# Kernel optimization log

Hardware: AMD Instinct MI355X
Metric: run time of the kernel (lower is better)

The kernel has to match this reference:

```python
import jax, jax.numpy as jnp
import numpy as np

NUM_HEADS = 8
DIM = 384


def conv2d(x, w, padding, groups=1):
    return jax.lax.conv_general_dilated(
        x, w, window_strides=(1, 1), padding=[(padding, padding), (padding, padding)],
        feature_group_count=groups, dimension_numbers=("NCHW", "OIHW", "NCHW"))


def setup_inputs() -> dict:
    key = jax.random.key(0)
    ks = jax.random.split(key, 6)
    d = DIM
    x = jax.random.normal(ks[0], (4, d, 128, 128), dtype=jnp.float32)
    w_qkv = jax.random.normal(ks[1], (3 * d, d, 1, 1), dtype=jnp.float32) * 0.05
    w_dw = jax.random.normal(ks[2], (3 * d, 1, 3, 3), dtype=jnp.float32) * 0.05
    w_proj = jax.random.normal(ks[3], (d, 2 * d, 1, 1), dtype=jnp.float32) * 0.05
    w_bs_pw = jax.random.normal(ks[4], (d, d, 1, 1), dtype=jnp.float32) * 0.05
    w_bs_dw = jax.random.normal(ks[5], (d, 1, 3, 3), dtype=jnp.float32) * 0.05
    return {"x": x, "w_qkv": w_qkv, "w_dw": w_dw, "w_proj": w_proj,
            "w_bs_pw": w_bs_pw, "w_bs_dw": w_bs_dw}


def reference(x, w_qkv, w_dw, w_proj, w_bs_pw, w_bs_dw):
    b, c, h, w = x.shape
    ch = c // NUM_HEADS
    # BSConvU branch: pointwise 1x1 then depthwise 3x3, then exact GELU
    y = conv2d(x, w_bs_pw, padding=0)
    y = conv2d(y, w_bs_dw, padding=1, groups=c)
    y = jax.nn.gelu(y, approximate=False)
    # qkv: 1x1 conv then depthwise 3x3
    qkv = conv2d(x, w_qkv, padding=0)
    qkv = conv2d(qkv, w_dw, padding=1, groups=3 * c)
    q, k, v = jnp.split(qkv, 3, axis=1)
    # b (head ch) h w -> b head ch (h w)
    def to_heads(t):
        return t.reshape(b, NUM_HEADS, ch, h * w)
    q, k, v = to_heads(q), to_heads(k), to_heads(v)
    # L2-normalize over spatial dim (torch F.normalize with eps=1e-12)
    q = q / jnp.maximum(jnp.linalg.norm(q, axis=-1, keepdims=True), 1e-12)
    k = k / jnp.maximum(jnp.linalg.norm(k, axis=-1, keepdims=True), 1e-12)
    scale = 1.0 / np.sqrt(ch).astype(np.float32)
    attn = jnp.einsum("bhcn,bhdn->bhcd", q, k) * scale  # channel-channel attention
    attn = jax.nn.softmax(attn, axis=-1)
    out = jnp.einsum("bhcd,bhdn->bhcn", attn, v)
    out = out.reshape(b, c, h, w)
    out = jnp.concatenate([out, y], axis=1)
    out = conv2d(out, w_proj, padding=0)
    return out
```

## Files before the change

### kernel.cpp

```cpp
#include <hip/hip_runtime.h>
#include <hip/hip_bf16.h>
#include <math.h>

typedef __hip_bfloat16 bf16;
typedef short bf16x8 __attribute__((ext_vector_type(8)));
typedef float f32x4 __attribute__((ext_vector_type(4)));

#define NPIX 16384

static __device__ __forceinline__ float ldv(float v) { return v; }
static __device__ __forceinline__ float ldv(bf16 v) { return __bfloat162float(v); }
static __device__ __forceinline__ float lds16(short s) {
    union { short s_; bf16 h; } u; u.s_ = s; return __bfloat162float(u.h);
}
template <typename T> static __device__ __forceinline__ T stv(float v);
template <> __device__ __forceinline__ float stv<float>(float v) { return v; }
template <> __device__ __forceinline__ bf16 stv<bf16>(float v) { return __float2bfloat16(v); }
static __device__ __forceinline__ short stv16(float v) {
    union { short s_; bf16 h; } u; u.h = __float2bfloat16(v); return u.s_;
}

static __device__ __forceinline__ unsigned pack2f(float a, float b) {
    union { bf16 h; unsigned short u; } ua, ub;
    ua.h = __float2bfloat16(a); ub.h = __float2bfloat16(b);
    return (unsigned)ua.u | ((unsigned)ub.u << 16);
}
static __device__ __forceinline__ unsigned packbb(unsigned short lo, unsigned short hi) {
    return (unsigned)lo | ((unsigned)hi << 16);
}

template <typename SrcT>
static __device__ __forceinline__ const SrcT* maprow(const SrcT* A, const SrcT* B, int k,
    int Ksplit, int agrp, int ags, int abss, int bgrp, int bgs, int bbs, int b)
{
    if (k < Ksplit) return A + (size_t)((k / agrp) * ags + b * abss + (k % agrp)) * NPIX;
    k -= Ksplit;
    return B + (size_t)((k / bgrp) * bgs + b * bbs + (k % bgrp)) * NPIX;
}

__global__ __launch_bounds__(256) void packw(const float* __restrict__ s,
                                             bf16* __restrict__ d, int n)
{
    int i = (blockIdx.x * 256 + threadIdx.x) * 8;
    if (i + 8 > n) return;
    float4 v0 = *(const float4*)(s + i);
    float4 v1 = *(const float4*)(s + i + 4);
    uint4 u;
    u.x = pack2f(v0.x, v0.y); u.y = pack2f(v0.z, v0.w);
    u.z = pack2f(v1.x, v1.y); u.w = pack2f(v1.z, v1.w);
    *(uint4*)(void*)(d + i) = u;
}

__global__ __launch_bounds__(256) void xpose(const float* __restrict__ x,
                                             bf16* __restrict__ xT)
{
    __shared__ short Ls[64 * 384];
    const int t = threadIdx.x;
    const int px0 = blockIdx.x * 64;
    const int b = blockIdx.y;
    const float* xb = x + (size_t)b * 384 * NPIX;

#pragma unroll 4
    for (int i = 0; i < 24; ++i) {
        int e = i * 256 + t;
        int ch = e >> 4, seg = e & 15;
        float4 v = *(const float4*)(xb + (size_t)ch * NPIX + px0 + seg * 4);
        const float* vp = (const float*)&v;
#pragma unroll
        for (int j = 0; j < 4; ++j) {
            int px = seg * 4 + j;
            int B = (ch >> 3) ^ ((px >> 2) & 7);
            Ls[px * 384 + B * 8 + (ch & 7)] = stv16(vp[j]);
        }
    }
    __syncthreads();

    const int lpx = t >> 2;
    const int m = (lpx >> 2) & 7;
    bf16* ob = xT + ((size_t)b * NPIX + px0 + lpx) * 384;
#pragma unroll
    for (int j = 0; j < 12; ++j) {
        int B = (t & 3) + j * 4;
        bf16x8 blk = *(const bf16x8*)&Ls[lpx * 384 + (B ^ m) * 8];
        *(bf16x8*)(void*)(ob + B * 8) = blk;
    }
}

__global__ __launch_bounds__(256) void xposeB(const bf16* __restrict__ src,
                                              bf16* __restrict__ dst)
{
    __shared__ short Ls[64 * 384];
    const int t = threadIdx.x;
    const int px0 = blockIdx.x * 64;
    const int b = blockIdx.y;
    const bf16* sb = src + (size_t)b * 384 * NPIX;

#pragma unroll 4
    for (int i = 0; i < 12; ++i) {
        int e = i * 256 + t;
        int ch = e >> 3, seg = e & 7;
        bf16x8 v = *(const bf16x8*)(const void*)(sb + (size_t)ch * NPIX + px0 + seg * 8);
#pragma unroll
        for (int j = 0; j < 8; ++j) {
            int px = seg * 8 + j;
            int B = (ch >> 3) ^ ((px >> 2) & 7);
            Ls[px * 384 + B * 8 + (ch & 7)] = v[j];
        }
    }
    __syncthreads();

    const int lpx = t >> 2;
    const int m = (lpx >> 2) & 7;
    bf16* ob = dst + ((size_t)b * NPIX + px0 + lpx) * 768 + 384;
#pragma unroll
    for (int j = 0; j < 12; ++j) {
        int B = (t & 3) + j * 4;
        bf16x8 blk = *(const bf16x8*)&Ls[lpx * 384 + (B ^ m) * 8];
        *(bf16x8*)(void*)(ob + B * 8) = blk;
    }
}

template <int BM, int K, typename OutT>
__global__ __launch_bounds__(256) void gemm3(
    const bf16* __restrict__ wp, int G, int wsA, int wrowMul,
    const bf16* __restrict__ bsrc,
    OutT* __restrict__ out, int osA, int obS,
    int bmCount, int nwg)
{
    constexpr int MT = BM / 16;
    constexpr int S  = K / 32;
    constexpr int ACH = BM * 4;
    __shared__ __align__(16) short As[2][BM * 40];
    __shared__ __align__(16) short Bs[2][128 * 40];

    const int t = threadIdx.x;
    const int gid = blockIdx.x;
    const int w = (gid & 7) * (nwg >> 3) + (gid >> 3);
    const int bm = w % bmCount, grp = w / bmCount;
    const int b = grp & 3, px0 = (grp >> 2) * 128;

    const int l = t & 63, wvid = t >> 6, l15 = l & 15, q = l >> 4;
    const int wr0 = bm * wrowMul;
    const size_t bRow0 = (size_t)b * NPIX + px0;

    const int e0 = t,        r0 = e0 >> 2, c0 = e0 & 3;
    const int e1 = t + 256,  r1 = e1 >> 2, c1 = e1 & 3;
    const bf16* apt0 = wp + (size_t)(wr0 + (r0 / G) * wsA + (r0 % G)) * K + c0 * 8;
    const bf16* apt1 = wp + (size_t)(wr0 + (r1 / G) * wsA + (r1 % G)) * K + c1 * 8;
    const int sA0 = r0 * 40 + c0 * 8, sA1 = r1 * 40 + c1 * 8;
    const bf16* apt2 = apt0; int sA2 = sA0; bool has2 = false;
    if constexpr (ACH > 512) {
        if (t < ACH - 512) {
            int e2 = t + 512, r2 = e2 >> 2, c2 = e2 & 3;
            apt2 = wp + (size_t)(wr0 + (r2 / G) * wsA + (r2 % G)) * K + c2 * 8;
            sA2 = r2 * 40 + c2 * 8;
            has2 = true;
        }
    }
    const bf16* bpt0 = bsrc + (bRow0 + r0) * K + c0 * 8;
    const bf16* bpt1 = bsrc + (bRow0 + r1) * K + c1 * 8;

    f32x4 acc[MT][2];
#pragma unroll
    for (int mt = 0; mt < MT; ++mt)
#pragma unroll
        for (int nt = 0; nt < 2; ++nt) acc[mt][nt] = (f32x4){0.f, 0.f, 0.f, 0.f};

    bf16x8 aR0, aR1, aR2, bR0, bR1;

    auto GLOADS = [&](int kk) {
        aR0 = *(const bf16x8*)(const void*)(apt0 + kk);
        aR1 = *(const bf16x8*)(const void*)(apt1 + kk);
        if constexpr (ACH > 512) { if (has2) aR2 = *(const bf16x8*)(const void*)(apt2 + kk); }
        bR0 = *(const bf16x8*)(const void*)(bpt0 + kk);
        bR1 = *(const bf16x8*)(const void*)(bpt1 + kk);
    };
    auto SSTORES = [&](int buf) {
        *(bf16x8*)&As[buf][sA0] = aR0;
        *(bf16x8*)&As[buf][sA1] = aR1;
        if constexpr (ACH > 512) { if (has2) *(bf16x8*)&As[buf][sA2] = aR2; }
        *(bf16x8*)&Bs[buf][sA0] = bR0;
        *(bf16x8*)&Bs[buf][sA1] = bR1;
    };

    GLOADS(0);
    SSTORES(0);
    __syncthreads();

#pragma unroll
    for (int s = 0; s < S; ++s) {
        const int cur = s & 1;
        if (s + 1 < S) GLOADS((s + 1) * 32);
        bf16x8 af[MT], bfv[2];
#pragma unroll
        for (int mt = 0; mt < MT; ++mt)
            af[mt] = *(const bf16x8*)&As[cur][(mt * 16 + l15) * 40 + q * 8];
#pragma unroll
        for (int nt = 0; nt < 2; ++nt)
            bfv[nt] = *(const bf16x8*)&Bs[cur][(wvid * 32 + nt * 16 + l15) * 40 + q * 8];
#pragma unroll
        for (int mt = 0; mt < MT; ++mt)
#pragma unroll
            for (int nt = 0; nt < 2; ++nt)
                acc[mt][nt] = __builtin_amdgcn_mfma_f32_16x16x32_bf16(
                    af[mt], bfv[nt], acc[mt][nt], 0, 0, 0);
        if (s + 1 < S) SSTORES(1 - cur);
        __syncthreads();
    }

    const int obase = bm * osA + b * obS;
#pragma unroll
    for (int mt = 0; mt < MT; ++mt)
#pragma unroll
        for (int nt = 0; nt < 2; ++nt)
#pragma unroll
            for (int r = 0; r < 4; ++r) {
                int row = obase + mt * 16 + q * 4 + r;
                int col = px0 + wvid * 32 + nt * 16 + l15;
                out[(size_t)row * NPIX + col] = stv<OutT>(acc[mt][nt][r]);
            }
}

template <typename SrcT, typename OutT>
__global__ __launch_bounds__(256) void gemm48(
    const SrcT* __restrict__ srcA, const SrcT* __restrict__ srcB, int Ksplit, int K,
    int agrp, int ags, int abss, int bgrp, int bgs, int bbs,
    const float* __restrict__ w, int wMod, int wsA, int wsB, int wrow0,
    OutT* __restrict__ out, int oMod, int osA, int osB, int obS, int orow0)
{
    __shared__ __align__(16) short As[2][48 * 40];
    __shared__ __align__(16) short Bs[2][128 * 40];

    const int t  = threadIdx.x;
    const int bm = blockIdx.x;
    const int p0 = blockIdx.y * 128;
    const int b  = blockIdx.z;

    const int l = t & 63, wvid = t >> 6, l15 = l & 15, q = l >> 4;
    const int c4 = t >> 4, rp = t & 15;

    const int wbase = wrow0 + (bm % wMod) * wsA + (bm / wMod) * wsB;

    f32x4 acc[3][2];
#pragma unroll
    for (int mt = 0; mt < 3; ++mt)
#pragma unroll
        for (int nt = 0; nt < 2; ++nt) acc[mt][nt] = (f32x4){0.f, 0.f, 0.f, 0.f};

    float aw[6];
    float fb[16];
    bf16x8 hA, hB;

    auto LOADA = [&](int k0) {
#pragma unroll
        for (int i = 0; i < 3; ++i) {
            int idx = t + i * 256, row = idx >> 4, kq = idx & 15;
            float2 v = *(const float2*)(w + (size_t)(wbase + row) * K + k0 + kq * 2);
            aw[2 * i] = v.x; aw[2 * i + 1] = v.y;
        }
    };
    auto STOREA = [&](int buf) {
#pragma unroll
        for (int i = 0; i < 3; ++i) {
            int idx = t + i * 256, row = idx >> 4, kq = idx & 15;
            *(unsigned*)&As[buf][row * 40 + kq * 2] = pack2f(aw[2 * i], aw[2 * i + 1]);
        }
    };
    auto LOADB = [&](int k0) {
        const SrcT* r0 = maprow(srcA, srcB, k0 + 2 * rp,     Ksplit, agrp, ags, abss, bgrp, bgs, bbs, b) + p0 + c4 * 8;
        const SrcT* r1 = maprow(srcA, srcB, k0 + 2 * rp + 1, Ksplit, agrp, ags, abss, bgrp, bgs, bbs, b) + p0 + c4 * 8;
        if constexpr (sizeof(SrcT) == 4) {
            float4 a0 = *(const float4*)r0, a1 = *(const float4*)(r0 + 4);
            float4 b0 = *(const float4*)r1, b1 = *(const float4*)(r1 + 4);
            fb[0] = a0.x; fb[1] = a0.y; fb[2] = a0.z; fb[3] = a0.w;
            fb[4] = a1.x; fb[5] = a1.y; fb[6] = a1.z; fb[7] = a1.w;
            fb[8] = b0.x; fb[9] = b0.y; fb[10] = b0.z; fb[11] = b0.w;
            fb[12] = b1.x; fb[13] = b1.y; fb[14] = b1.z; fb[15] = b1.w;
        } else {
            hA = *(const bf16x8*)(const void*)r0;
            hB = *(const bf16x8*)(const void*)r1;
        }
    };
    auto STOREB = [&](int buf) {
#pragma unroll
        for (int j = 0; j < 8; ++j) {
            unsigned d;
            if constexpr (sizeof(SrcT) == 4) d = pack2f(fb[j], fb[8 + j]);
            else d = packbb((unsigned short)hA[j], (unsigned short)hB[j]);
            *(unsigned*)&Bs[buf][(c4 * 8 + j) * 40 + rp * 2] = d;
        }
    };

    LOADA(0); LOADB(0);
    STOREA(0); STOREB(0);
    const int S = K / 32;
    for (int s = 0; s < S; ++s) {
        const int cur = s & 1;
        __syncthreads();
        if (s + 1 < S) { LOADA((s + 1) * 32); LOADB((s + 1) * 32); }
        bf16x8 af[3], bfr[2];
#pragma unroll
        for (int mt = 0; mt < 3; ++mt)
            af[mt] = *(const bf16x8*)&As[cur][(mt * 16 + l15) * 40 + q * 8];
#pragma unroll
        for (int nt = 0; nt < 2; ++nt)
            bfr[nt] = *(const bf16x8*)&Bs[cur][(wvid * 32 + nt * 16 + l15) * 40 + q * 8];
#pragma unroll
        for (int mt = 0; mt < 3; ++mt)
#pragma unroll
            for (int nt = 0; nt < 2; ++nt)
                acc[mt][nt] = __builtin_amdgcn_mfma_f32_16x16x32_bf16(
                    af[mt], bfr[nt], acc[mt][nt], 0, 0, 0);
        if (s + 1 < S) { STOREA(1 - cur); STOREB(1 - cur); }
    }

    const int obase = orow0 + (bm % oMod) * osA + (bm / oMod) * osB + b * obS;
#pragma unroll
    for (int mt = 0; mt < 3; ++mt)
#pragma unroll
        for (int nt = 0; nt < 2; ++nt)
#pragma unroll
            for (int r = 0; r < 4; ++r) {
                int row = obase + mt * 16 + q * 4 + r;
                int col = p0 + wvid * 32 + nt * 16 + l15;
                out[(size_t)row * NPIX + col] = stv<OutT>(acc[mt][nt][r]);
            }
}

__global__ __launch_bounds__(256) void dw3x3v(
    const bf16* __restrict__ in, const float* __restrict__ w, bf16* __restrict__ out,
    int isQkv, int whofs, int inB, int ig, int outB, int og, int obase, int applyGelu)
{
    const int t = threadIdx.x;
    const int g = blockIdx.x * 256 + t;
    const int c = blockIdx.y;
    const int b = blockIdx.z;
    const int y = g >> 4;
    const int x0 = (g & 15) * 8;

    int inRow, wch, outRow;
    if (isQkv) {
        int h = c / 144, r = c - h * 144;
        inRow  = h * ig + b * inB + r;
        wch    = (r / 48) * 384 + h * 48 + whofs + (r % 48);
        outRow = h * og + b * outB + r + obase;
    } else {
        inRow = b * inB + c; wch = c; outRow = b * outB + c;
    }

    const bf16* ib = in + (size_t)inRow * NPIX;
    float wv[9];
#pragma unroll
    for (int i = 0; i < 9; ++i) wv[i] = w[wch * 9 + i];

    float vv[3][10];
#pragma unroll
    for (int dy = 0; dy < 3; ++dy) {
        int yy = y + dy - 1;
        if (yy < 0 || yy > 127) {
#pragma unroll
            for (int j = 0; j < 10; ++j) vv[dy][j] = 0.f;
        } else {
            const bf16* rb = ib + yy * 128;
            bf16x8 m = *(const bf16x8*)(const void*)(rb + x0);
#pragma unroll
            for (int j = 0; j < 8; ++j) vv[dy][j + 1] = lds16(m[j]);
            vv[dy][0] = (x0 > 0)   ? ldv(rb[x0 - 1]) : 0.f;
            vv[dy][9] = (x0 < 120) ? ldv(rb[x0 + 8]) : 0.f;
        }
    }
    bf16x8 res;
#pragma unroll
    for (int j = 0; j < 8; ++j) {
        float a = 0.f;
#pragma unroll
        for (int dy = 0; dy < 3; ++dy)
#pragma unroll
            for (int dx = 0; dx < 3; ++dx)
                a += wv[dy * 3 + dx] * vv[dy][j + dx];
        if (applyGelu) a = 0.5f * a * (1.0f + erff(a * 0.70710678118654752f));
        res[j] = stv16(a);
    }
    *(bf16x8*)(void*)(out + (size_t)outRow * NPIX + y * 128 + x0) = res;
}

__global__ __launch_bounds__(256) void l2norm_v(const bf16* __restrict__ qkvd,
                                                float* __restrict__ inv, int NBH)
{
    const int id = blockIdx.x;
    const int which = id / (NBH * 48);
    const int rem = id - which * NBH * 48;
    const int bh = rem / 48, c = rem - bh * 48;
    const bf16* base = qkvd + (size_t)(bh * 144 + which * 48 + c) * NPIX;

    float s = 0.f;
#pragma unroll
    for (int it = 0; it < 8; ++it) {
        bf16x8 v = *(const bf16x8*)(const void*)(base + ((size_t)threadIdx.x + it * 256) * 8);
#pragma unroll
        for (int j = 0; j < 8; ++j) { float f = lds16(v[j]); s += f * f; }
    }
#pragma unroll
    for (int off = 32; off; off >>= 1) s += __shfl_down(s, off, 64);
    __shared__ float partial[4];
    if ((threadIdx.x & 63) == 0) partial[threadIdx.x >> 6] = s;
    __syncthreads();
    if (threadIdx.x == 0) {
        float tt = partial[0] + partial[1] + partial[2] + partial[3];
        inv[(which * NBH + bh) * 48 + c] = 1.0f / fmaxf(sqrtf(tt), 1e-12f);
    }
}

__global__ __launch_bounds__(256) void qk_mfma(const bf16* __restrict__ qkvd,
                                               float* __restrict__ lp, int NBH, int pxs)
{
    const int bh = blockIdx.x;
    const int wvid = threadIdx.x >> 6;
    const int slice = blockIdx.y * 4 + wvid;
    const int l = threadIdx.x & 63, l15 = l & 15, q = l >> 4;

    const bf16* qb = qkvd + (size_t)(bh * 144) * NPIX;
    const bf16* kb = qb + (size_t)48 * NPIX;

    f32x4 acc[3][3];
#pragma unroll
    for (int mt = 0; mt < 3; ++mt)
#pragma unroll
        for (int nt = 0; nt < 3; ++nt) acc[mt][nt] = (f32x4){0.f, 0.f, 0.f, 0.f};

    const int pbeg = slice * pxs;
    for (int kk = 0; kk < pxs; kk += 32) {
        const int pc = pbeg + kk + q * 8;
        bf16x8 af[3], bfv[3];
#pragma unroll
        for (int mt = 0; mt < 3; ++mt)
            af[mt] = *(const bf16x8*)(const void*)(qb + (size_t)(mt * 16 + l15) * NPIX + pc);
#pragma unroll
        for (int nt = 0; nt < 3; ++nt)
            bfv[nt] = *(const bf16x8*)(const void*)(kb + (size_t)(nt * 16 + l15) * NPIX + pc);
#pragma unroll
        for (int mt = 0; mt < 3; ++mt)
#pragma unroll
            for (int nt = 0; nt < 3; ++nt)
                acc[mt][nt] = __builtin_amdgcn_mfma_f32_16x16x32_bf16(
                    af[mt], bfv[nt], acc[mt][nt], 0, 0, 0);
    }
    float* o = lp + ((size_t)slice * NBH + bh) * 2304;
#pragma unroll
    for (int mt = 0; mt < 3; ++mt)
#pragma unroll
        for (int nt = 0; nt < 3; ++nt)
#pragma unroll
            for (int r = 0; r < 4; ++r)
                o[(mt * 16 + q * 4 + r) * 48 + nt * 16 + l15] = acc[mt][nt][r];
}

__global__ __launch_bounds__(256) void logit_reduce(const float* __restrict__ lp,
                                                    const float* __restrict__ inv,
                                                    float* __restrict__ L,
                                                    int NBH, int NSL)
{
    const int blk = blockIdx.x;
    const int bh = blk / 9, chunk = blk - bh * 9;
    const int e = chunk * 256 + threadIdx.x;
    float s = 0.f;
    for (int sl = 0; sl < NSL; ++sl)
        s += lp[((size_t)sl * NBH + bh) * 2304 + e];
    const int i = e / 48, j = e - i * 48;
    L[(size_t)bh * 2304 + e] =
        s * 0.14433756729740643f * inv[bh * 48 + i] * inv[(NBH + bh) * 48 + j];
}

__global__ __launch_bounds__(256) void softmax48b(const float* __restrict__ Lg,
                                                  bf16* __restrict__ a_bf)
{
    const int bh = blockIdx.x, t = threadIdx.x;
    __shared__ float L[2304];
    for (int e = t; e < 2304; e += 256) L[e] = Lg[(size_t)bh * 2304 + e];
    __syncthreads();
    if (t < 48) {
        float m = -1e30f;
#pragma unroll
        for (int j = 0; j < 48; ++j) m = fmaxf(m, L[t * 48 + j]);
        float e_[48]; float ssum = 0.f;
#pragma unroll
        for (int j = 0; j < 48; ++j) { e_[j] = expf(L[t * 48 + j] - m); ssum += e_[j]; }
        float r = 1.f / ssum;
        bf16* ab = a_bf + (size_t)bh * 3072 + t * 64;
#pragma unroll
        for (int j = 0; j < 48; ++j) ab[j] = stv<bf16>(e_[j] * r);
#pragma unroll
        for (int j = 48; j < 64; ++j) ab[j] = stv<bf16>(0.f);
    }
}

__global__ __launch_bounds__(256) void softmax48(const float* __restrict__ lp,
                                                 const float* __restrict__ inv,
                                                 bf16* __restrict__ a_bf, int NBH, int NSL)
{
    const int bh = blockIdx.x, t = threadIdx.x;
    __shared__ float L[2304];
    for (int e = t; e < 2304; e += 256) {
        float s = 0.f;
        for (int sl = 0; sl < NSL; ++sl) s += lp[((size_t)sl * NBH + bh) * 2304 + e];
        int i = e / 48, j = e - i * 48;
        L[e] = s * 0.14433756729740643f * inv[bh * 48 + i] * inv[(NBH + bh) * 48 + j];
    }
    __syncthreads();
    if (t < 48) {
        float m = -1e30f;
#pragma unroll
        for (int j = 0; j < 48; ++j) m = fmaxf(m, L[t * 48 + j]);
        float e_[48]; float ssum = 0.f;
#pragma unroll
        for (int j = 0; j < 48; ++j) { e_[j] = expf(L[t * 48 + j] - m); ssum += e_[j]; }
        float r = 1.f / ssum;
        bf16* ab = a_bf + (size_t)bh * 3072 + t * 64;
#pragma unroll
        for (int j = 0; j < 48; ++j) ab[j] = stv<bf16>(e_[j] * r);
#pragma unroll
        for (int j = 48; j < 64; ++j) ab[j] = stv<bf16>(0.f);
    }
}

__global__ __launch_bounds__(256) void av_mfma(const bf16* __restrict__ a_bf,
                                               const bf16* __restrict__ qkvd,
                                               bf16* __restrict__ out, int obase, int oS)
{
    __shared__ __align__(16) short Bs[128 * 72];
    const int t = threadIdx.x;
    const int px0 = blockIdx.x * 128;
    const int bh = blockIdx.y;
    const int l = t & 63, wvid = t >> 6, l15 = l & 15, q = l >> 4;
    const int c4 = t >> 4, rp = t & 15;

    const bf16* ab = a_bf + (size_t)bh * 3072;
    bf16x8 af[3][2];
#pragma unroll
    for (int mt = 0; mt < 3; ++mt)
#pragma unroll
        for (int kq = 0; kq < 2; ++kq)
            af[mt][kq] = *(const bf16x8*)(const void*)(ab + (mt * 16 + l15) * 64 + kq * 32 + q * 8);

    const bf16* vb = qkvd + (size_t)(bh * 144 + 96) * NPIX;
    bf16x8 vr[4];
#pragma unroll
    for (int jj = 0; jj < 4; ++jj) {
        int j = rp * 4 + jj; int jc = j < 48 ? j : 47;
        vr[jj] = *(const bf16x8*)(const void*)(vb + (size_t)jc * NPIX + px0 + c4 * 8);
    }
#pragma unroll
    for (int j = 0; j < 8; ++j) {
        *(unsigned*)&Bs[(c4 * 8 + j) * 72 + rp * 4]     = packbb((unsigned short)vr[0][j], (unsigned short)vr[1][j]);
        *(unsigned*)&Bs[(c4 * 8 + j) * 72 + rp * 4 + 2] = packbb((unsigned short)vr[2][j], (unsigned short)vr[3][j]);
    }
    __syncthreads();

    f32x4 acc[3][2];
#pragma unroll
    for (int mt = 0; mt < 3; ++mt)
#pragma unroll
        for (int nt = 0; nt < 2; ++nt) acc[mt][nt] = (f32x4){0.f, 0.f, 0.f, 0.f};

    bf16x8 bfv[2][2];
#pragma unroll
    for (int nt = 0; nt < 2; ++nt)
#pragma unroll
        for (int kq = 0; kq < 2; ++kq)
            bfv[nt][kq] = *(const bf16x8*)&Bs[(wvid * 32 + nt * 16 + l15) * 72 + kq * 32 + q * 8];
#pragma unroll
    for (int kq = 0; kq < 2; ++kq)
#pragma unroll
        for (int mt = 0; mt < 3; ++mt)
#pragma unroll
            for (int nt = 0; nt < 2; ++nt)
                acc[mt][nt] = __builtin_amdgcn_mfma_f32_16x16x32_bf16(
                    af[mt][kq], bfv[nt][kq], acc[mt][nt], 0, 0, 0);
#pragma unroll
    for (int mt = 0; mt < 3; ++mt)
#pragma unroll
        for (int nt = 0; nt < 2; ++nt)
#pragma unroll
            for (int r = 0; r < 4; ++r) {
                int row = obase + bh * oS + mt * 16 + q * 4 + r;
                int col = px0 + wvid * 32 + nt * 16 + l15;
                out[(size_t)row * NPIX + col] = stv<bf16>(acc[mt][nt][r]);
            }
}

__global__ __launch_bounds__(256) void av_mfma2(const bf16* __restrict__ a_bf,
                                                const bf16* __restrict__ qkvd,
                                                bf16* __restrict__ pxT)
{
    __shared__ __align__(16) short Bs[128 * 72];
    const int t = threadIdx.x;
    const int px0 = blockIdx.x * 128;
    const int bh = blockIdx.y;
    const int l = t & 63, wvid = t >> 6, l15 = l & 15, q = l >> 4;
    const int c4 = t >> 4, rp = t & 15;

    const bf16* ab = a_bf + (size_t)bh * 3072;
    bf16x8 af[3][2];
#pragma unroll
    for (int mt = 0; mt < 3; ++mt)
#pragma unroll
        for (int kq = 0; kq < 2; ++kq)
            af[mt][kq] = *(const bf16x8*)(const void*)(ab + (mt * 16 + l15) * 64 + kq * 32 + q * 8);

    const bf16* vb = qkvd + (size_t)(bh * 144 + 96) * NPIX;
    bf16x8 vr[4];
#pragma unroll
    for (int jj = 0; jj < 4; ++jj) {
        int j = rp * 4 + jj; int jc = j < 48 ? j : 47;
        vr[jj] = *(const bf16x8*)(const void*)(vb + (size_t)jc * NPIX + px0 + c4 * 8);
    }
#pragma unroll
    for (int j = 0; j < 8; ++j) {
        *(unsigned*)&Bs[(c4 * 8 + j) * 72 + rp * 4]     = packbb((unsigned short)vr[0][j], (unsigned short)vr[1][j]);
        *(unsigned*)&Bs[(c4 * 8 + j) * 72 + rp * 4 + 2] = packbb((unsigned short)vr[2][j], (unsigned short)vr[3][j]);
    }
    __syncthreads();

    f32x4 acc[3][2];
#pragma unroll
    for (int mt = 0; mt < 3; ++mt)
#pragma unroll
        for (int nt = 0; nt < 2; ++nt) acc[mt][nt] = (f32x4){0.f, 0.f, 0.f, 0.f};

    bf16x8 bfv[2][2];
#pragma unroll
    for (int nt = 0; nt < 2; ++nt)
#pragma unroll
        for (int kq = 0; kq < 2; ++kq)
            bfv[nt][kq] = *(const bf16x8*)&Bs[(wvid * 32 + nt * 16 + l15) * 72 + kq * 32 + q * 8];
#pragma unroll
    for (int kq = 0; kq < 2; ++kq)
#pragma unroll
        for (int mt = 0; mt < 3; ++mt)
#pragma unroll
            for (int nt = 0; nt < 2; ++nt)
                acc[mt][nt] = __builtin_amdgcn_mfma_f32_16x16x32_bf16(
                    af[mt][kq], bfv[nt][kq], acc[mt][nt], 0, 0, 0);

    __syncthreads();
#pragma unroll
    for (int mt = 0; mt < 3; ++mt)
#pragma unroll
        for (int nt = 0; nt < 2; ++nt) {
            int pxl = wvid * 32 + nt * 16 + l15;
#pragma unroll
            for (int r = 0; r < 2; ++r)
                *(unsigned*)&Bs[pxl * 48 + mt * 16 + q * 4 + r * 2] =
                    pack2f(acc[mt][nt][2 * r], acc[mt][nt][2 * r + 1]);
        }
    __syncthreads();

    const int h = bh >> 2, bb = bh & 3;
    const int pxl = t >> 1, half = t & 1;
    bf16* ob = pxT + ((size_t)bb * NPIX + px0 + pxl) * 768 + h * 48 + half * 24;
#pragma unroll
    for (int j = 0; j < 3; ++j)
        *(bf16x8*)(void*)(ob + j * 8) = *(const bf16x8*)&Bs[pxl * 48 + half * 24 + j * 8];
}

extern "C" void kernel_launch(void* const* d_in, const int* in_sizes, int n_in,
                              void* d_out, int out_size, void* d_ws, size_t ws_size,
                              hipStream_t stream) {
    const float* x       = (const float*)d_in[0];
    const float* w_qkv   = (const float*)d_in[1];
    const float* w_dw    = (const float*)d_in[2];
    const float* w_proj  = (const float*)d_in[3];
    const float* w_bs_pw = (const float*)d_in[4];
    const float* w_bs_dw = (const float*)d_in[5];
    float* out = (float*)d_out;
    bf16* y1 = (bf16*)d_out;

    const size_t SZQ = 150994944ull;
    const size_t SZH = 18874368ull;
    const size_t SZY = 50331648ull;
    const size_t SZPXT = 100663296ull;
    char* ws = (char*)d_ws;
    dim3 blk(256);

    if (ws_size >= 371404800ull) {
        bf16* qkvp = (bf16*)ws;
        bf16* pxT  = (bf16*)ws;
        bf16* wprojp = (bf16*)(ws + SZPXT);
        float* Lbuf  = (float*)(ws + SZPXT + 1048576ull);
        bf16* qkvd = (bf16*)(ws + SZQ);
        bf16* xT   = (bf16*)(ws + 2 * SZQ);
        bf16* yg   = xT;
        float* lp  = (float*)(ws + 2 * SZQ + SZY);
        bf16* wqkvp = (bf16*)lp;
        bf16* wbsp  = (bf16*)((char*)lp + 884736ull);
        bf16* abf  = (bf16*)(ws + 2 * SZQ + SZY + 18874368ull);
        float* inv = (float*)(ws + 2 * SZQ + SZY + 18874368ull + 196608ull);

        packw<<<dim3(216), blk, 0, stream>>>(w_qkv, wqkvp, 442368);
        packw<<<dim3(72), blk, 0, stream>>>(w_bs_pw, wbsp, 147456);
        xpose<<<dim3(256, 4), blk, 0, stream>>>(x, xT);
        gemm3<144, 384, bf16><<<dim3(4096), blk, 0, stream>>>(
            wqkvp, 48, 384, 48, xT, qkvp, 576, 144, 8, 4096);
        dw3x3v<<<dim3(8, 1152, 4), blk, 0, stream>>>(
            qkvp, w_dw, qkvd, 1, 0, 144, 576, 144, 576, 0, 0);
        packw<<<dim3(144), blk, 0, stream>>>(w_proj, wprojp, 294912);
        gemm3<128, 384, bf16><<<dim3(1536), blk, 0, stream>>>(
            wbsp, 128, 0, 128, xT, y1, 128, 384, 3, 1536);
        dw3x3v<<<dim3(8, 384, 4), blk, 0, stream>>>(
            y1, w_bs_dw, yg, 0, 0, 384, 0, 384, 0, 0, 1);
        xposeB<<<dim3(256, 4), blk, 0, stream>>>(yg, pxT);
        l2norm_v<<<dim3(2 * 32 * 48), blk, 0, stream>>>(qkvd, inv, 32);
        qk_mfma<<<dim3(32, 16), blk, 0, stream>>>(qkvd, lp, 32, 256);
        logit_reduce<<<dim3(32 * 9), blk, 0, stream>>>(lp, inv, Lbuf, 32, 64);
        softmax48b<<<dim3(32), blk, 0, stream>>>(Lbuf, abf);
        av_mfma2<<<dim3(128, 32), blk, 0, stream>>>(abf, qkvd, pxT);
        gemm3<128, 768, float><<<dim3(1536), blk, 0, stream>>>(
            wprojp, 128, 0, 128, pxT, out, 128, 384, 3, 1536);
    } else if (ws_size >= 239284224ull) {
        bf16* qkvd = (bf16*)ws;
        bf16* qph  = (bf16*)(ws + SZQ);
        bf16* yg   = (bf16*)(ws + SZQ + SZH);
        float* lp  = (float*)(ws + SZQ + SZH + SZY);
        bf16* abf  = (bf16*)(ws + SZQ + SZH + SZY + 18874368ull);
        float* inv = (float*)(ws + SZQ + SZH + SZY + 18874368ull + 196608ull);

        for (int h = 0; h < 8; ++h) {
            gemm48<float, bf16><<<dim3(3, 128, 4), blk, 0, stream>>>(
                x, x, 384, 384, 384, 0, 384, 384, 0, 384,
                w_qkv, 3, 384, 48, h * 48, qph, 3, 48, 0, 144, 0);
            dw3x3v<<<dim3(8, 144, 4), blk, 0, stream>>>(
                qph, w_dw, qkvd, 1, h * 48, 144, 0, 144, 0, h * 576, 0);
        }
        l2norm_v<<<dim3(2 * 32 * 48), blk, 0, stream>>>(qkvd, inv, 32);
        qk_mfma<<<dim3(32, 16), blk, 0, stream>>>(qkvd, lp, 32, 256);
        softmax48<<<dim3(32), blk, 0, stream>>>(lp, inv, abf, 32, 64);
        gemm48<float, bf16><<<dim3(8, 128, 4), blk, 0, stream>>>(
            x, x, 384, 384, 384, 0, 384, 384, 0, 384,
            w_bs_pw, 1, 0, 48, 0, y1, 1, 0, 48, 384, 0);
        dw3x3v<<<dim3(8, 384, 4), blk, 0, stream>>>(
            y1, w_bs_dw, yg, 0, 0, 384, 0, 384, 0, 0, 1);
        av_mfma<<<dim3(128, 32), blk, 0, stream>>>(abf, qkvd, qkvd, 0, 144);
        gemm48<bf16, float><<<dim3(8, 128, 4), blk, 0, stream>>>(
            qkvd, yg, 384, 768, 48, 576, 144, 384, 0, 384,
            w_proj, 1, 0, 48, 0, out, 1, 0, 48, 384, 0);
    } else {
        bf16* qph   = (bf16*)ws;
        bf16* qkvdh = (bf16*)(ws + SZH);
        bf16* yg    = (bf16*)(ws + 2 * SZH);
        bf16* attn  = (bf16*)(ws + 2 * SZH + SZY);
        float* lp   = (float*)(ws + 2 * SZH + 2 * SZY);
        bf16* abf   = (bf16*)(ws + 2 * SZH + 2 * SZY + 1179648ull);
        float* inv  = (float*)(ws + 2 * SZH + 2 * SZY + 1179648ull + 24576ull);

        gemm48<float, bf16><<<dim3(8, 128, 4), blk, 0, stream>>>(
            x, x, 384, 384, 384, 0, 384, 384, 0, 384,
            w_bs_pw, 1, 0, 48, 0, y1, 1, 0, 48, 384, 0);
        dw3x3v<<<dim3(8, 384, 4), blk, 0, stream>>>(
            y1, w_bs_dw, yg, 0, 0, 384, 0, 384, 0, 0, 1);
        for (int h = 0; h < 8; ++h) {
            gemm48<float, bf16><<<dim3(3, 128, 4), blk, 0, stream>>>(
                x, x, 384, 384, 384, 0, 384, 384, 0, 384,
                w_qkv, 3, 384, 48, h * 48, qph, 3, 48, 0, 144, 0);
            dw3x3v<<<dim3(8, 144, 4), blk, 0, stream>>>(
                qph, w_dw, qkvdh, 1, h * 48, 144, 0, 144, 0, 0, 0);
            l2norm_v<<<dim3(2 * 4 * 48), blk, 0, stream>>>(qkvdh, inv, 4);
            qk_mfma<<<dim3(4, 8), blk, 0, stream>>>(qkvdh, lp, 4, 512);
            softmax48<<<dim3(4), blk, 0, stream>>>(lp, inv, abf, 4, 32);
            av_mfma<<<dim3(128, 4), blk, 0, stream>>>(abf, qkvdh, attn, h * 48, 384);
        }
        gemm48<bf16, float><<<dim3(8, 128, 4), blk, 0, stream>>>(
            attn, yg, 384, 768, 384, 0, 384, 384, 0, 384,
            w_proj, 1, 0, 48, 0, out, 1, 0, 48, 384, 0);
    }
}
```

Baseline: 625.3 us.

## Fuse L2 sum-of-squares into depthwise conv, two rows per thread

The depthwise 3x3 kernel now computes two output rows per thread, reusing the loaded input rows, and gets horizontal halo values by lane shuffles instead of extra scalar loads. In the main path it also accumulates per-channel sum of squares for q and k through a block reduction and an atomicAdd, so the separate l2norm pass that re-read qkvd is removed. Two small kernels are added, one to zero the accumulator and one to turn it into inverse norms. The accumulator is placed as scratch in the tail of the output buffer, which the final projection later overwrites. This adds atomics, and the sum of squares is taken on fp32 values before bf16 rounding.

```diff
diff --git a/kernel.cpp b/kernel.cpp
--- a/kernel.cpp
+++ b/kernel.cpp
@@ -49,6 +49,19 @@
     u.x = pack2f(v0.x, v0.y); u.y = pack2f(v0.z, v0.w);
     u.z = pack2f(v1.x, v1.y); u.w = pack2f(v1.z, v1.w);
     *(uint4*)(void*)(d + i) = u;
+}
+
+__global__ __launch_bounds__(256) void zerok(float* __restrict__ p, int n)
+{
+    int i = blockIdx.x * 256 + threadIdx.x;
+    if (i < n) p[i] = 0.f;
+}
+
+__global__ __launch_bounds__(256) void invk(const float* __restrict__ ss,
+                                            float* __restrict__ inv, int n)
+{
+    int i = blockIdx.x * 256 + threadIdx.x;
+    if (i < n) inv[i] = 1.f / fmaxf(sqrtf(ss[i]), 1e-12f);
 }
 
 __global__ __launch_bounds__(256) void xpose(const float* __restrict__ x,
@@ -327,23 +340,26 @@
             }
 }
 
-__global__ __launch_bounds__(256) void dw3x3v(
+__global__ __launch_bounds__(256) void dw3x3s(
     const bf16* __restrict__ in, const float* __restrict__ w, bf16* __restrict__ out,
-    int isQkv, int whofs, int inB, int ig, int outB, int og, int obase, int applyGelu)
+    int isQkv, int whofs, int inB, int ig, int outB, int og, int obase,
+    int applyGelu, float* __restrict__ sumsq, int nbh)
 {
     const int t = threadIdx.x;
     const int g = blockIdx.x * 256 + t;
     const int c = blockIdx.y;
     const int b = blockIdx.z;
-    const int y = g >> 4;
+    const int y0 = (g >> 4) * 2;
     const int x0 = (g & 15) * 8;
-
-    int inRow, wch, outRow;
+    const int xl = t & 15;
+
+    int inRow, wch, outRow, nidx = -1;
     if (isQkv) {
         int h = c / 144, r = c - h * 144;
         inRow  = h * ig + b * inB + r;
         wch    = (r / 48) * 384 + h * 48 + whofs + (r % 48);
         outRow = h * og + b * outB + r + obase;
+        if (r < 96) nidx = ((r / 48) * nbh + (h * 4 + b)) * 48 + (r % 48);
     } else {
         inRow = b * inB + c; wch = c; outRow = b * outB + c;
     }
@@ -353,35 +369,48 @@
 #pragma unroll
     for (int i = 0; i < 9; ++i) wv[i] = w[wch * 9 + i];
 
-    float vv[3][10];
-#pragma unroll
-    for (int dy = 0; dy < 3; ++dy) {
-        int yy = y + dy - 1;
-        if (yy < 0 || yy > 127) {
-#pragma unroll
-            for (int j = 0; j < 10; ++j) vv[dy][j] = 0.f;
-        } else {
-            const bf16* rb = ib + yy * 128;
-            bf16x8 m = *(const bf16x8*)(const void*)(rb + x0);
-#pragma unroll
-            for (int j = 0; j < 8; ++j) vv[dy][j + 1] = lds16(m[j]);
-            vv[dy][0] = (x0 > 0)   ? ldv(rb[x0 - 1]) : 0.f;
-            vv[dy][9] = (x0 < 120) ? ldv(rb[x0 + 8]) : 0.f;
-        }
-    }
-    bf16x8 res;
-#pragma unroll
-    for (int j = 0; j < 8; ++j) {
-        float a = 0.f;
-#pragma unroll
-        for (int dy = 0; dy < 3; ++dy)
-#pragma unroll
-            for (int dx = 0; dx < 3; ++dx)
-                a += wv[dy * 3 + dx] * vv[dy][j + dx];
-        if (applyGelu) a = 0.5f * a * (1.0f + erff(a * 0.70710678118654752f));
-        res[j] = stv16(a);
-    }
-    *(bf16x8*)(void*)(out + (size_t)outRow * NPIX + y * 128 + x0) = res;
+    float vv[4][10];
+#pragma unroll
+    for (int dy = 0; dy < 4; ++dy) {
+        int yy = y0 + dy - 1;
+        bf16x8 m = (bf16x8){0, 0, 0, 0, 0, 0, 0, 0};
+        if (yy >= 0 && yy <= 127)
+            m = *(const bf16x8*)(const void*)(ib + yy * 128 + x0);
+#pragma unroll
+        for (int j = 0; j < 8; ++j) vv[dy][j + 1] = lds16(m[j]);
+        float lf = __shfl_up(vv[dy][8], 1, 16);
+        float rf = __shfl_down(vv[dy][1], 1, 16);
+        vv[dy][0] = (xl == 0)  ? 0.f : lf;
+        vv[dy][9] = (xl == 15) ? 0.f : rf;
+    }
+
+    float ssum = 0.f;
+#pragma unroll
+    for (int oy = 0; oy < 2; ++oy) {
+        bf16x8 res;
+#pragma unroll
+        for (int j = 0; j < 8; ++j) {
+            float a = 0.f;
+#pragma unroll
+            for (int dy = 0; dy < 3; ++dy)
+#pragma unroll
+                for (int dx = 0; dx < 3; ++dx)
+                    a += wv[dy * 3 + dx] * vv[oy + dy][j + dx];
+            if (applyGelu) a = 0.5f * a * (1.0f + erff(a * 0.70710678118654752f));
+            ssum += a * a;
+            res[j] = stv16(a);
+        }
+        *(bf16x8*)(void*)(out + (size_t)outRow * NPIX + (y0 + oy) * 128 + x0) = res;
+    }
+
+    if (sumsq != nullptr && nidx >= 0) {
+#pragma unroll
+        for (int off = 32; off; off >>= 1) ssum += __shfl_down(ssum, off, 64);
+        __shared__ float sp[4];
+        if ((t & 63) == 0) sp[t >> 6] = ssum;
+        __syncthreads();
+        if (t == 0) atomicAdd(&sumsq[nidx], sp[0] + sp[1] + sp[2] + sp[3]);
+    }
 }
 
 __global__ __launch_bounds__(256) void l2norm_v(const bf16* __restrict__ qkvd,
@@ -695,21 +724,23 @@
         bf16* wbsp  = (bf16*)((char*)lp + 884736ull);
         bf16* abf  = (bf16*)(ws + 2 * SZQ + SZY + 18874368ull);
         float* inv = (float*)(ws + 2 * SZQ + SZY + 18874368ull + 196608ull);
+        float* sumsq = (float*)((char*)d_out + 100663296ull - 16384ull);
 
         packw<<<dim3(216), blk, 0, stream>>>(w_qkv, wqkvp, 442368);
         packw<<<dim3(72), blk, 0, stream>>>(w_bs_pw, wbsp, 147456);
         xpose<<<dim3(256, 4), blk, 0, stream>>>(x, xT);
         gemm3<144, 384, bf16><<<dim3(4096), blk, 0, stream>>>(
             wqkvp, 48, 384, 48, xT, qkvp, 576, 144, 8, 4096);
-        dw3x3v<<<dim3(8, 1152, 4), blk, 0, stream>>>(
-            qkvp, w_dw, qkvd, 1, 0, 144, 576, 144, 576, 0, 0);
+        zerok<<<dim3(12), blk, 0, stream>>>(sumsq, 3072);
+        dw3x3s<<<dim3(4, 1152, 4), blk, 0, stream>>>(
+            qkvp, w_dw, qkvd, 1, 0, 144, 576, 144, 576, 0, 0, sumsq, 32);
+        invk<<<dim3(12), blk, 0, stream>>>(sumsq, inv, 3072);
         packw<<<dim3(144), blk, 0, stream>>>(w_proj, wprojp, 294912);
         gemm3<128, 384, bf16><<<dim3(1536), blk, 0, stream>>>(
             wbsp, 128, 0, 128, xT, y1, 128, 384, 3, 1536);
-        dw3x3v<<<dim3(8, 384, 4), blk, 0, stream>>>(
-            y1, w_bs_dw, yg, 0, 0, 384, 0, 384, 0, 0, 1);
+        dw3x3s<<<dim3(4, 384, 4), blk, 0, stream>>>(
+            y1, w_bs_dw, yg, 0, 0, 384, 0, 384, 0, 0, 1, nullptr, 0);
         xposeB<<<dim3(256, 4), blk, 0, stream>>>(yg, pxT);
-        l2norm_v<<<dim3(2 * 32 * 48), blk, 0, stream>>>(qkvd, inv, 32);
         qk_mfma<<<dim3(32, 16), blk, 0, stream>>>(qkvd, lp, 32, 256);
         logit_reduce<<<dim3(32 * 9), blk, 0, stream>>>(lp, inv, Lbuf, 32, 64);
         softmax48b<<<dim3(32), blk, 0, stream>>>(Lbuf, abf);
@@ -728,8 +759,8 @@
             gemm48<float, bf16><<<dim3(3, 128, 4), blk, 0, stream>>>(
                 x, x, 384, 384, 384, 0, 384, 384, 0, 384,
                 w_qkv, 3, 384, 48, h * 48, qph, 3, 48, 0, 144, 0);
-            dw3x3v<<<dim3(8, 144, 4), blk, 0, stream>>>(
-                qph, w_dw, qkvd, 1, h * 48, 144, 0, 144, 0, h * 576, 0);
+            dw3x3s<<<dim3(4, 144, 4), blk, 0, stream>>>(
+                qph, w_dw, qkvd, 1, h * 48, 144, 0, 144, 0, h * 576, 0, nullptr, 0);
         }
         l2norm_v<<<dim3(2 * 32 * 48), blk, 0, stream>>>(qkvd, inv, 32);
         qk_mfma<<<dim3(32, 16), blk, 0, stream>>>(qkvd, lp, 32, 256);
@@ -737,8 +768,8 @@
         gemm48<float, bf16><<<dim3(8, 128, 4), blk, 0, stream>>>(
             x, x, 384, 384, 384, 0, 384, 384, 0, 384,
             w_bs_pw, 1, 0, 48, 0, y1, 1, 0, 48, 384, 0);
-        dw3x3v<<<dim3(8, 384, 4), blk, 0, stream>>>(
-            y1, w_bs_dw, yg, 0, 0, 384, 0, 384, 0, 0, 1);
+        dw3x3s<<<dim3(4, 384, 4), blk, 0, stream>>>(
+            y1, w_bs_dw, yg, 0, 0, 384, 0, 384, 0, 0, 1, nullptr, 0);
         av_mfma<<<dim3(128, 32), blk, 0, stream>>>(abf, qkvd, qkvd, 0, 144);
         gemm48<bf16, float><<<dim3(8, 128, 4), blk, 0, stream>>>(
             qkvd, yg, 384, 768, 48, 576, 144, 384, 0, 384,
@@ -755,14 +786,14 @@
         gemm48<float, bf16><<<dim3(8, 128, 4), blk, 0, stream>>>(
             x, x, 384, 384, 384, 0, 384, 384, 0, 384,
             w_bs_pw, 1, 0, 48, 0, y1, 1, 0, 48, 384, 0);
-        dw3x3v<<<dim3(8, 384, 4), blk, 0, stream>>>(
-            y1, w_bs_dw, yg, 0, 0, 384, 0, 384, 0, 0, 1);
+        dw3x3s<<<dim3(4, 384, 4), blk, 0, stream>>>(
+            y1, w_bs_dw, yg, 0, 0, 384, 0, 384, 0, 0, 1, nullptr, 0);
         for (int h = 0; h < 8; ++h) {
             gemm48<float, bf16><<<dim3(3, 128, 4), blk, 0, stream>>>(
                 x, x, 384, 384, 384, 0, 384, 384, 0, 384,
                 w_qkv, 3, 384, 48, h * 48, qph, 3, 48, 0, 144, 0);
-            dw3x3v<<<dim3(8, 144, 4), blk, 0, stream>>>(
-                qph, w_dw, qkvdh, 1, h * 48, 144, 0, 144, 0, 0, 0);
+            dw3x3s<<<dim3(4, 144, 4), blk, 0, stream>>>(
+                qph, w_dw, qkvdh, 1, h * 48, 144, 0, 144, 0, 0, 0, nullptr, 0);
             l2norm_v<<<dim3(2 * 4 * 48), blk, 0, stream>>>(qkvdh, inv, 4);
             qk_mfma<<<dim3(4, 8), blk, 0, stream>>>(qkvdh, lp, 4, 512);
             softmax48<<<dim3(4), blk, 0, stream>>>(lp, inv, abf, 4, 32);
```

New measurement: 582.5 us. -6.8%, faster.
